# Kernel optimization log

Measured on AMD Instinct MI355X. Metric: run time of the kernel, lower is better.

Reference implementation:

```python
import jax, jax.numpy as jnp
import numpy as np


def setup_inputs() -> dict:
    key = jax.random.key(0)
    k1, k2 = jax.random.split(key)
    B, N, D = 8, 1024, 64
    y = jax.random.normal(k1, (B, N, D), dtype=jnp.float32)
    y_hat = jax.random.normal(k2, (B, N, D), dtype=jnp.float32)
    return {"y": y, "y_hat": y_hat}


def reference(y, y_hat):
    # StochLoss with dim=1: repeat element i along dim 1 (i+1) times,
    # square, then unbiased variance over all elements (torch .var() default).
    n = y.shape[1]
    counts = np.arange(1, n + 1)              # linspace(1, n, n).int() == 1..n
    total = n * (n + 1) // 2                  # static expanded length
    diff = y - y_hat                          # [B, N, D]
    w = jnp.repeat(diff, counts, axis=1, total_repeat_length=total)  # [B, n(n+1)/2, D]
    errors = w * w
    loss = jnp.var(errors, ddof=1)            # unbiased, matches torch.var()
    return loss
```

## Files before the change

kernel.cpp:

```cpp
#include <hip/hip_runtime.h>

#define NBLK 256
#define NTHR 256

__global__ __launch_bounds__(NTHR) void stoch_partial(
    const float4* __restrict__ y,
    const float4* __restrict__ yh,
    double* __restrict__ ws,
    int n4)
{
    int tid = blockIdx.x * blockDim.x + threadIdx.x;
    double s = 0.0, s2 = 0.0;

    for (int idx = tid; idx < n4; idx += NBLK * NTHR) {
        float4 a = y[idx];
        float4 b = yh[idx];
        int i = (idx >> 4) & 1023;
        double w = (double)(i + 1);
        float d0 = a.x - b.x, d1 = a.y - b.y, d2 = a.z - b.z, d3 = a.w - b.w;
        float e0 = d0 * d0, e1 = d1 * d1, e2 = d2 * d2, e3 = d3 * d3;
        double se  = (double)e0 + (double)e1 + (double)e2 + (double)e3;
        double se2 = (double)e0 * e0 + (double)e1 * e1
                   + (double)e2 * e2 + (double)e3 * e3;
        s  += w * se;
        s2 += w * se2;
    }

    for (int off = 32; off > 0; off >>= 1) {
        s  += __shfl_down(s,  off, 64);
        s2 += __shfl_down(s2, off, 64);
    }

    __shared__ double sh[2][NTHR / 64];
    int wave = threadIdx.x >> 6;
    int lane = threadIdx.x & 63;
    if (lane == 0) { sh[0][wave] = s; sh[1][wave] = s2; }
    __syncthreads();

    if (threadIdx.x == 0) {
        double ts = 0.0, ts2 = 0.0;
        #pragma unroll
        for (int wv = 0; wv < NTHR / 64; ++wv) { ts += sh[0][wv]; ts2 += sh[1][wv]; }
        ws[2 * blockIdx.x]     = ts;
        ws[2 * blockIdx.x + 1] = ts2;
    }
}

__global__ __launch_bounds__(NTHR) void stoch_final(
    const double* __restrict__ ws,
    float* __restrict__ out,
    double M)
{
    int tid = threadIdx.x;
    double s  = ws[2 * tid];
    double s2 = ws[2 * tid + 1];

    for (int off = 32; off > 0; off >>= 1) {
        s  += __shfl_down(s,  off, 64);
        s2 += __shfl_down(s2, off, 64);
    }

    __shared__ double sh[2][NTHR / 64];
    int wave = tid >> 6;
    int lane = tid & 63;
    if (lane == 0) { sh[0][wave] = s; sh[1][wave] = s2; }
    __syncthreads();

    if (tid == 0) {
        double S = 0.0, S2 = 0.0;
        #pragma unroll
        for (int wv = 0; wv < NTHR / 64; ++wv) { S += sh[0][wv]; S2 += sh[1][wv]; }
        double var = (S2 - S * S / M) / (M - 1.0);
        out[0] = (float)var;
    }
}

extern "C" void kernel_launch(void* const* d_in, const int* in_sizes, int n_in,
                              void* d_out, int out_size, void* d_ws, size_t ws_size,
                              hipStream_t stream) {
    const float4* y  = (const float4*)d_in[0];
    const float4* yh = (const float4*)d_in[1];
    double* ws = (double*)d_ws;
    float* out = (float*)d_out;

    const int n_elem = in_sizes[0];
    const int n4 = n_elem / 4;

    const double B = 8.0, N = 1024.0, D = 64.0;
    const double M = B * (N * (N + 1.0) * 0.5) * D;

    stoch_partial<<<NBLK, NTHR, 0, stream>>>(y, yh, ws, n4);
    stoch_final<<<1, NTHR, 0, stream>>>(ws, out, M);
}
```

Before: 11.18 us.

## Fuse partial and final reductions into one cooperative kernel with grid sync

Merges the two reduction kernels into a single cooperative launch, using a grid-wide barrier before block 0 reduces the per-block partial sums and writes the variance. The grid-stride loop becomes a fixed two-iteration unrolled loop per thread. This removes the second kernel launch and its gap, but adds the cost of a grid sync and of cooperative launch setup.

```diff
diff --git a/kernel.cpp b/kernel.cpp
--- a/kernel.cpp
+++ b/kernel.cpp
@@ -1,40 +1,52 @@
 #include <hip/hip_runtime.h>
+#include <hip/hip_cooperative_groups.h>
+
+namespace cg = cooperative_groups;
 
 #define NBLK 256
 #define NTHR 256
+#define PER_THREAD 2
 
-__global__ __launch_bounds__(NTHR) void stoch_partial(
+__global__ __launch_bounds__(NTHR) void stoch_fused(
     const float4* __restrict__ y,
     const float4* __restrict__ yh,
     double* __restrict__ ws,
-    int n4)
+    float* __restrict__ out,
+    double M, int n4)
 {
-    int tid = blockIdx.x * blockDim.x + threadIdx.x;
+    cg::grid_group grid = cg::this_grid();
+
+    int tid = blockIdx.x * NTHR + threadIdx.x;
     double s = 0.0, s2 = 0.0;
 
-    for (int idx = tid; idx < n4; idx += NBLK * NTHR) {
-        float4 a = y[idx];
-        float4 b = yh[idx];
-        int i = (idx >> 4) & 1023;
-        double w = (double)(i + 1);
-        float d0 = a.x - b.x, d1 = a.y - b.y, d2 = a.z - b.z, d3 = a.w - b.w;
-        float e0 = d0 * d0, e1 = d1 * d1, e2 = d2 * d2, e3 = d3 * d3;
-        double se  = (double)e0 + (double)e1 + (double)e2 + (double)e3;
-        double se2 = (double)e0 * e0 + (double)e1 * e1
-                   + (double)e2 * e2 + (double)e3 * e3;
-        s  += w * se;
-        s2 += w * se2;
+    #pragma unroll
+    for (int p = 0; p < PER_THREAD; ++p) {
+        int idx = tid + p * (NBLK * NTHR);
+        if (idx < n4) {
+            float4 a = y[idx];
+            float4 b = yh[idx];
+            int i = (idx >> 4) & 1023;
+            double w = (double)(i + 1);
+            float d0 = a.x - b.x, d1 = a.y - b.y, d2 = a.z - b.z, d3 = a.w - b.w;
+            float e0 = d0 * d0, e1 = d1 * d1, e2 = d2 * d2, e3 = d3 * d3;
+            s  += w * ((double)e0 + (double)e1 + (double)e2 + (double)e3);
+            s2 += w * ((double)e0 * e0 + (double)e1 * e1
+                     + (double)e2 * e2 + (double)e3 * e3);
+        }
     }
 
+    #pragma unroll
     for (int off = 32; off > 0; off >>= 1) {
         s  += __shfl_down(s,  off, 64);
         s2 += __shfl_down(s2, off, 64);
     }
 
     __shared__ double sh[2][NTHR / 64];
-    int wave = threadIdx.x >> 6;
-    int lane = threadIdx.x & 63;
-    if (lane == 0) { sh[0][wave] = s; sh[1][wave] = s2; }
+    {
+        int wave = threadIdx.x >> 6;
+        int lane = threadIdx.x & 63;
+        if (lane == 0) { sh[0][wave] = s; sh[1][wave] = s2; }
+    }
     __syncthreads();
 
     if (threadIdx.x == 0) {
@@ -44,34 +56,31 @@
         ws[2 * blockIdx.x]     = ts;
         ws[2 * blockIdx.x + 1] = ts2;
     }
-}
 
-__global__ __launch_bounds__(NTHR) void stoch_final(
-    const double* __restrict__ ws,
-    float* __restrict__ out,
-    double M)
-{
-    int tid = threadIdx.x;
-    double s  = ws[2 * tid];
-    double s2 = ws[2 * tid + 1];
+    grid.sync();
 
-    for (int off = 32; off > 0; off >>= 1) {
-        s  += __shfl_down(s,  off, 64);
-        s2 += __shfl_down(s2, off, 64);
-    }
+    if (blockIdx.x == 0) {
+        double a  = ws[2 * threadIdx.x];
+        double b2 = ws[2 * threadIdx.x + 1];
 
-    __shared__ double sh[2][NTHR / 64];
-    int wave = tid >> 6;
-    int lane = tid & 63;
-    if (lane == 0) { sh[0][wave] = s; sh[1][wave] = s2; }
-    __syncthreads();
+        #pragma unroll
+        for (int off = 32; off > 0; off >>= 1) {
+            a  += __shfl_down(a,  off, 64);
+            b2 += __shfl_down(b2, off, 64);
+        }
 
-    if (tid == 0) {
-        double S = 0.0, S2 = 0.0;
-        #pragma unroll
-        for (int wv = 0; wv < NTHR / 64; ++wv) { S += sh[0][wv]; S2 += sh[1][wv]; }
-        double var = (S2 - S * S / M) / (M - 1.0);
-        out[0] = (float)var;
+        int wave = threadIdx.x >> 6;
+        int lane = threadIdx.x & 63;
+        if (lane == 0) { sh[0][wave] = a; sh[1][wave] = b2; }
+        __syncthreads();
+
+        if (threadIdx.x == 0) {
+            double S = 0.0, S2 = 0.0;
+            #pragma unroll
+            for (int wv = 0; wv < NTHR / 64; ++wv) { S += sh[0][wv]; S2 += sh[1][wv]; }
+            double var = (S2 - S * S / M) / (M - 1.0);
+            out[0] = (float)var;
+        }
     }
 }
 
@@ -83,12 +92,14 @@
     double* ws = (double*)d_ws;
     float* out = (float*)d_out;
 
-    const int n_elem = in_sizes[0];
-    const int n4 = n_elem / 4;
+    int n_elem = in_sizes[0];
+    int n4 = n_elem / 4;
 
     const double B = 8.0, N = 1024.0, D = 64.0;
-    const double M = B * (N * (N + 1.0) * 0.5) * D;
+    double M = B * (N * (N + 1.0) * 0.5) * D;
 
-    stoch_partial<<<NBLK, NTHR, 0, stream>>>(y, yh, ws, n4);
-    stoch_final<<<1, NTHR, 0, stream>>>(ws, out, M);
+    void* args[] = { (void*)&y, (void*)&yh, (void*)&ws, (void*)&out,
+                     (void*)&M, (void*)&n4 };
+    hipLaunchCooperativeKernel((const void*)stoch_fused,
+                               dim3(NBLK), dim3(NTHR), args, 0, stream);
 }
```

Result: slower. 35.87 us (+221.0%).
